# Kernel tuning notes

Hardware: AMD Instinct MI355X
Metric: run time of the kernel (lower is better)

The kernel has to match this reference:

```python
import jax, jax.numpy as jnp
import numpy as np

D = 1024
NH = 16
DH = D // NH
B = 2
N = 2048
EPS = 1e-5


def setup_inputs() -> dict:
    key = jax.random.key(0)
    ks = jax.random.split(key, 12)
    s = 0.02
    return {
        "x": jax.random.normal(ks[0], (B, N, D), jnp.float32),
        "Wq": jax.random.normal(ks[1], (D, D), jnp.float32) * s,
        "Wk": jax.random.normal(ks[2], (D, D), jnp.float32) * s,
        "Wv": jax.random.normal(ks[3], (D, D), jnp.float32) * s,
        "Wo": jax.random.normal(ks[4], (D, D), jnp.float32) * s,
        "bo": jnp.zeros((D,), jnp.float32),
        "ln1_scale": jnp.ones((D,), jnp.float32),
        "ln1_shift": jnp.zeros((D,), jnp.float32),
        "ln2_scale": jnp.ones((D,), jnp.float32),
        "ln2_shift": jnp.zeros((D,), jnp.float32),
        "W1": jax.random.normal(ks[5], (4 * D, D), jnp.float32) * s,
        "b1": jnp.zeros((4 * D,), jnp.float32),
        "W2": jax.random.normal(ks[6], (D, 4 * D), jnp.float32) * s,
        "b2": jnp.zeros((D,), jnp.float32),
    }


def _layernorm(x, scale, shift):
    mean = jnp.mean(x, axis=-1, keepdims=True)
    var = jnp.mean(jnp.square(x - mean), axis=-1, keepdims=True)  # unbiased=False
    return scale * ((x - mean) / jnp.sqrt(var + EPS)) + shift


def _gelu(x):
    c = jnp.sqrt(jnp.asarray(2.0 / jnp.pi, x.dtype))
    return 0.5 * x * (1.0 + jnp.tanh(c * (x + 0.044715 * x * x * x)))


def reference(x, Wq, Wk, Wv, Wo, bo, ln1_scale, ln1_shift, ln2_scale, ln2_shift, W1, b1, W2, b2):
    Bx, Nx, d = x.shape
    # pre-MHA LN
    h = _layernorm(x, ln1_scale, ln1_shift)
    # projections (torch Linear: y = h @ W.T), no bias for Wq/Wk/Wv
    q = (h @ Wq.T).reshape(Bx, Nx, NH, DH).transpose(0, 2, 1, 3)  # [B,nh,N,dh]
    k = (h @ Wk.T).reshape(Bx, Nx, NH, DH).transpose(0, 2, 1, 3)
    v = (h @ Wv.T).reshape(Bx, Nx, NH, DH).transpose(0, 2, 1, 3)
    s = jnp.einsum("bhnd,bhmd->bhnm", q, k)  # [B,nh,N,N]
    causal = jnp.tril(jnp.ones((Nx, Nx), bool))
    s = jnp.where(causal, s, -jnp.inf)
    p = jax.nn.softmax(s / jnp.sqrt(jnp.asarray(DH, s.dtype)), axis=-1)
    pv = jnp.einsum("bhnm,bhmd->bhnd", p, v)
    pv = pv.transpose(0, 2, 1, 3).reshape(Bx, Nx, d)
    attn = pv @ Wo.T + bo
    x = x + attn  # residual (dropout is identity, dpo=0)
    # pre-FFN LN + FFN
    h = _layernorm(x, ln2_scale, ln2_shift)
    h = _gelu(h @ W1.T + b1)
    h = h @ W2.T + b2
    return x + h
```

## Files before the change

kernel.cpp:

```cpp
#include <hip/hip_runtime.h>
#include <hip/hip_bf16.h>
#include <math.h>

#define Dmod   1024
#define NHmod  16
#define DHmod  64
#define Bmod   2
#define Nmod   2048
#define Mrows  (Bmod * Nmod)
#define FF     (4 * Dmod)
#define EPSLN  1e-5f

typedef __attribute__((ext_vector_type(8))) short bf16x8;
typedef __attribute__((ext_vector_type(4))) float f32x4;
typedef unsigned short ushort_t;
typedef unsigned int uint_t;

#define MFMA16x16x32(a, b, c) __builtin_amdgcn_mfma_f32_16x16x32_bf16((a), (b), (c), 0, 0, 0)

#define AS1 __attribute__((address_space(1)))
#define AS3 __attribute__((address_space(3)))

__device__ __forceinline__ void gload_lds16(const ushort_t* g, ushort_t* l) {
    __builtin_amdgcn_global_load_lds((const AS1 uint_t*)(const void*)g,
                                     (AS3 uint_t*)(void*)l, 16, 0, 0);
}

__device__ __forceinline__ ushort_t f2bf(float f) {
    union { float f; uint_t u; } v; v.f = f;
    uint_t r = v.u + 0x7FFFu + ((v.u >> 16) & 1u);
    return (ushort_t)(r >> 16);
}

__device__ __forceinline__ float bf2f(uint_t u) {
    union { float f; uint_t u; } v; v.u = u << 16;
    return v.f;
}

__global__ __launch_bounds__(256) void cvt_kernel(const float* __restrict__ Wq, const float* __restrict__ Wk,
                                                  const float* __restrict__ Wv, const float* __restrict__ Wo,
                                                  const float* __restrict__ W1, const float* __restrict__ W2,
                                                  ushort_t* __restrict__ qkv, ushort_t* __restrict__ wo,
                                                  ushort_t* __restrict__ w1, ushort_t* __restrict__ w2) {
    int u = blockIdx.x * 256 + threadIdx.x;
    const float* src; ushort_t* dst; int i;
    float scale = 1.0f;
    if (u < 393216) {
        if (u < 131072)      { src = Wq; dst = qkv;           i = u; scale = 0.125f; }
        else if (u < 262144) { src = Wk; dst = qkv + 1048576; i = u - 131072; }
        else                 { src = Wv; dst = qkv + 2097152; i = u - 262144; }
    } else if (u < 524288)   { src = Wo; dst = wo; i = u - 393216; }
    else if (u < 1048576)    { src = W1; dst = w1; i = u - 524288; }
    else                     { src = W2; dst = w2; i = u - 1048576; }
    float4 a = ((const float4*)src)[2 * i];
    float4 b = ((const float4*)src)[2 * i + 1];
    uint4 o;
    o.x = (uint_t)f2bf(a.x * scale) | ((uint_t)f2bf(a.y * scale) << 16);
    o.y = (uint_t)f2bf(a.z * scale) | ((uint_t)f2bf(a.w * scale) << 16);
    o.z = (uint_t)f2bf(b.x * scale) | ((uint_t)f2bf(b.y * scale) << 16);
    o.w = (uint_t)f2bf(b.z * scale) | ((uint_t)f2bf(b.w * scale) << 16);
    ((uint4*)dst)[i] = o;
}

__global__ __launch_bounds__(256) void ln_bf_kernel(const float* __restrict__ x,
                                                    const float* __restrict__ scale,
                                                    const float* __restrict__ shift,
                                                    ushort_t* __restrict__ out) {
    int row = blockIdx.x;
    const float4* xr = (const float4*)(x + (size_t)row * Dmod);
    float4 v = xr[threadIdx.x];
    float s  = v.x + v.y + v.z + v.w;
    float s2 = v.x*v.x + v.y*v.y + v.z*v.z + v.w*v.w;

    __shared__ float rs[8], rs2[8];
    #pragma unroll
    for (int o = 32; o; o >>= 1) { s += __shfl_down(s, o); s2 += __shfl_down(s2, o); }
    int wave = threadIdx.x >> 6, lane = threadIdx.x & 63;
    if (lane == 0) { rs[wave] = s; rs2[wave] = s2; }
    __syncthreads();
    if (threadIdx.x == 0) {
        rs[0]  = rs[0] + rs[1] + rs[2] + rs[3];
        rs2[0] = rs2[0] + rs2[1] + rs2[2] + rs2[3];
    }
    __syncthreads();
    float mean = rs[0] * (1.0f / Dmod);
    float var  = rs2[0] * (1.0f / Dmod) - mean * mean;
    float rstd = rsqrtf(var + EPSLN);

    float4 sc = ((const float4*)scale)[threadIdx.x];
    float4 sh = ((const float4*)shift)[threadIdx.x];
    uint2 o;
    o.x = (uint_t)f2bf(sc.x * (v.x - mean) * rstd + sh.x) |
          ((uint_t)f2bf(sc.y * (v.y - mean) * rstd + sh.y) << 16);
    o.y = (uint_t)f2bf(sc.z * (v.z - mean) * rstd + sh.z) |
          ((uint_t)f2bf(sc.w * (v.w - mean) * rstd + sh.w) << 16);
    ((uint2*)(out + (size_t)row * Dmod))[threadIdx.x] = o;
}

__device__ __forceinline__ float gelu_f(float x) {
    const float c = 0.7978845608028654f;
    float u = c * (x + 0.044715f * x * x * x);
    return x / (1.0f + __expf(-2.0f * u));
}

#define DSR(D, A, OFF) asm volatile("ds_read_b128 %0, %1 offset:" OFF : "=v"(D) : "v"(A))
#define SB0 __builtin_amdgcn_sched_barrier(0)
#define BARR __builtin_amdgcn_s_barrier()
#define LGKM0 asm volatile("s_waitcnt lgkmcnt(0)" ::)

#define MMQ0 \
  acc[0][0]=MFMA16x16x32(a0,b0,acc[0][0]); acc[1][0]=MFMA16x16x32(a1,b0,acc[1][0]); \
  acc[2][0]=MFMA16x16x32(a2,b0,acc[2][0]); acc[3][0]=MFMA16x16x32(a3,b0,acc[3][0]); \
  acc[0][1]=MFMA16x16x32(a0,b1,acc[0][1]); acc[1][1]=MFMA16x16x32(a1,b1,acc[1][1]); \
  acc[2][1]=MFMA16x16x32(a2,b1,acc[2][1]); acc[3][1]=MFMA16x16x32(a3,b1,acc[3][1]); \
  acc[0][2]=MFMA16x16x32(a0,b2,acc[0][2]); acc[1][2]=MFMA16x16x32(a1,b2,acc[1][2]); \
  acc[2][2]=MFMA16x16x32(a2,b2,acc[2][2]); acc[3][2]=MFMA16x16x32(a3,b2,acc[3][2]); \
  acc[0][3]=MFMA16x16x32(a0,b3,acc[0][3]); acc[1][3]=MFMA16x16x32(a1,b3,acc[1][3]); \
  acc[2][3]=MFMA16x16x32(a2,b3,acc[2][3]); acc[3][3]=MFMA16x16x32(a3,b3,acc[3][3]);
#define MMQ4 \
  acc[4][0]=MFMA16x16x32(a0,b0,acc[4][0]); acc[5][0]=MFMA16x16x32(a1,b0,acc[5][0]); \
  acc[6][0]=MFMA16x16x32(a2,b0,acc[6][0]); acc[7][0]=MFMA16x16x32(a3,b0,acc[7][0]); \
  acc[4][1]=MFMA16x16x32(a0,b1,acc[4][1]); acc[5][1]=MFMA16x16x32(a1,b1,acc[5][1]); \
  acc[6][1]=MFMA16x16x32(a2,b1,acc[6][1]); acc[7][1]=MFMA16x16x32(a3,b1,acc[7][1]); \
  acc[4][2]=MFMA16x16x32(a0,b2,acc[4][2]); acc[5][2]=MFMA16x16x32(a1,b2,acc[5][2]); \
  acc[6][2]=MFMA16x16x32(a2,b2,acc[6][2]); acc[7][2]=MFMA16x16x32(a3,b2,acc[7][2]); \
  acc[4][3]=MFMA16x16x32(a0,b3,acc[4][3]); acc[5][3]=MFMA16x16x32(a1,b3,acc[5][3]); \
  acc[6][3]=MFMA16x16x32(a2,b3,acc[6][3]); acc[7][3]=MFMA16x16x32(a3,b3,acc[7][3]);

template <int MODE>
__global__ __launch_bounds__(512, 2) void gemm256(const ushort_t* __restrict__ A,
                                                  const ushort_t* __restrict__ W,
                                                  const float* __restrict__ bias,
                                                  void* __restrict__ Cv,
                                                  int M, int Nout, int K, int KS,
                                                  int GN, int GM) {
    __shared__ ushort_t Ab[32768];
    __shared__ ushort_t Bb[32768];
    int tid = threadIdx.x;
    int w  = tid >> 6, l = tid & 63;
    int li = l & 15,  g = l >> 4;
    int wm = w >> 2,  wn = w & 3;

    int xcd = blockIdx.x & 7;
    int c   = blockIdx.x >> 3;
    int RN = GN >> 2, RM = GM >> 1;
    int rsz = RN * RM;
    int bz = c / rsz;
    int r  = c - bz * rsz;
    int bm = (xcd >> 2) * RM + r / RN;
    int bn = (xcd & 3) * RN + r % RN;

    int lc   = (l & 7) ^ (l >> 3);
    int sgr  = w * 32 + 2 * (l >> 3) + (lc >> 2);
    int colo = (lc & 3) * 8;
    const ushort_t* sA0 = A + (size_t)(bm * 256 + sgr) * K + bz * KS + colo;
    const ushort_t* sA1 = sA0 + (size_t)16 * K;
    const ushort_t* sB0 = W + (size_t)(bn * 256 + sgr) * K + bz * KS + colo;
    const ushort_t* sB1 = sB0 + (size_t)16 * K;

    uint_t chunkpos = (uint_t)(((((li & 1) << 2) + g) ^ (li >> 1)) << 4);
    uint_t aBase = (uint_t)(uintptr_t)(&Ab[0]) + (uint_t)(wm * 8192 + (li >> 1) * 128) + chunkpos;
    uint_t bBase = (uint_t)(uintptr_t)(&Bb[0]) + (uint_t)(wn * 4096 + (li >> 1) * 128) + chunkpos;

    f32x4 acc[8][4];
    #pragma unroll
    for (int i = 0; i < 8; i++)
        #pragma unroll
        for (int j = 0; j < 4; j++) acc[i][j] = (f32x4){0.f, 0.f, 0.f, 0.f};

    const int NT = KS >> 6;

    {
        ushort_t* dA = &Ab[0] + w * 1024;
        ushort_t* dB = &Bb[0] + w * 1024;
        gload_lds16(sA0,      dA);        gload_lds16(sA1,      dA + 512);
        gload_lds16(sB0,      dB);        gload_lds16(sB1,      dB + 512);
        gload_lds16(sA0 + 32, dA + 8192); gload_lds16(sA1 + 32, dA + 8192 + 512);
        gload_lds16(sB0 + 32, dB + 8192); gload_lds16(sB1 + 32, dB + 8192 + 512);
    }
    asm volatile("s_waitcnt vmcnt(4)" ::);
    SB0; BARR;

    for (int t = 0; t < NT; ++t) {
        int d = t & 1;
        bool pf = (t + 1 < NT);
        int kn = (t + 1) * 64;
        uint_t aAddr = aBase + (uint_t)(d * 32768);
        uint_t bAddr = bBase + (uint_t)(d * 32768);
        ushort_t* dA = &Ab[0] + (d ^ 1) * 16384 + w * 1024;
        ushort_t* dB = &Bb[0] + (d ^ 1) * 16384 + w * 1024;
        bf16x8 a0, a1, a2, a3, b0, b1, b2, b3;

        DSR(a0, aAddr, "0");    DSR(a1, aAddr, "1024");
        DSR(a2, aAddr, "2048"); DSR(a3, aAddr, "3072");
        DSR(b0, bAddr, "0");    DSR(b1, bAddr, "1024");
        DSR(b2, bAddr, "2048"); DSR(b3, bAddr, "3072");
        if (pf) { gload_lds16(sA0 + kn, dA); gload_lds16(sA1 + kn, dA + 512); }
        SB0; BARR; LGKM0; SB0;
        __builtin_amdgcn_s_setprio(1);
        MMQ0
        __builtin_amdgcn_s_setprio(0);
        SB0; BARR;

        DSR(a0, aAddr, "4096"); DSR(a1, aAddr, "5120");
        DSR(a2, aAddr, "6144"); DSR(a3, aAddr, "7168");
        if (pf) { gload_lds16(sB0 + kn, dB); gload_lds16(sB1 + kn, dB + 512); }
        SB0; BARR; LGKM0; SB0;
        __builtin_amdgcn_s_setprio(1);
        MMQ4
        __builtin_amdgcn_s_setprio(0);
        if (pf) { asm volatile("s_waitcnt vmcnt(4)" ::); }
        else    { asm volatile("s_waitcnt vmcnt(0)" ::); }
        SB0; BARR;

        DSR(a0, aAddr, "16384"); DSR(a1, aAddr, "17408");
        DSR(a2, aAddr, "18432"); DSR(a3, aAddr, "19456");
        DSR(b0, bAddr, "16384"); DSR(b1, bAddr, "17408");
        DSR(b2, bAddr, "18432"); DSR(b3, bAddr, "19456");
        if (pf) { gload_lds16(sA0 + kn + 32, dA + 8192); gload_lds16(sA1 + kn + 32, dA + 8192 + 512); }
        SB0; BARR; LGKM0; SB0;
        __builtin_amdgcn_s_setprio(1);
        MMQ0
        __builtin_amdgcn_s_setprio(0);
        SB0; BARR;

        DSR(a0, aAddr, "20480"); DSR(a1, aAddr, "21504");
        DSR(a2, aAddr, "22528"); DSR(a3, aAddr, "23552");
        if (pf) { gload_lds16(sB0 + kn + 32, dB + 8192); gload_lds16(sB1 + kn + 32, dB + 8192 + 512); }
        SB0; BARR; LGKM0; SB0;
        __builtin_amdgcn_s_setprio(1);
        MMQ4
        __builtin_amdgcn_s_setprio(0);
        asm volatile("s_waitcnt vmcnt(4)" ::);
        SB0; BARR;
    }

    #pragma unroll
    for (int fm = 0; fm < 8; fm++) {
        #pragma unroll
        for (int fn = 0; fn < 4; fn++) {
            int nn = bn * 256 + wn * 64 + fn * 16 + li;
            int mB = bm * 256 + wm * 128 + (fm >> 2) * 64 + (fm & 3) * 16 + g * 4;
            if (MODE == 0) {
                int which = nn >> 10, col = nn & 1023;
                int h = col >> 6, dd = col & 63;
                int b = mB >> 11, n0 = mB & (Nmod - 1);
                ushort_t* C = (ushort_t*)Cv;
                if (which == 2) {
                    uint2 pk;
                    pk.x = (uint_t)f2bf(acc[fm][fn][0]) | ((uint_t)f2bf(acc[fm][fn][1]) << 16);
                    pk.y = (uint_t)f2bf(acc[fm][fn][2]) | ((uint_t)f2bf(acc[fm][fn][3]) << 16);
                    *(uint2*)(C + 8388608u + (((size_t)(b * NHmod + h)) * DHmod + dd) * Nmod + n0) = pk;
                } else {
                    #pragma unroll
                    for (int r2 = 0; r2 < 4; r2++) {
                        size_t idx = (size_t)which * 4194304u +
                                     (((size_t)(b * NHmod + h)) * Nmod + n0 + r2) * DHmod + dd;
                        C[idx] = f2bf(acc[fm][fn][r2]);
                    }
                }
            } else if (MODE == 2) {
                ushort_t* C = (ushort_t*)Cv;
                #pragma unroll
                for (int r2 = 0; r2 < 4; r2++)
                    C[(size_t)(mB + r2) * Nout + nn] = f2bf(gelu_f(acc[fm][fn][r2] + bias[nn]));
            } else {
                ushort_t* P = (ushort_t*)Cv + (size_t)bz * M * Nout;
                #pragma unroll
                for (int r2 = 0; r2 < 4; r2++)
                    P[(size_t)(mB + r2) * Nout + nn] = f2bf(acc[fm][fn][r2]);
            }
        }
    }
}

template <int MODE, int BN>
__global__ __launch_bounds__(256) void bgemm(const ushort_t* __restrict__ A,
                                             const ushort_t* __restrict__ W,
                                             const float* __restrict__ bias,
                                             const float* __restrict__ resid,
                                             void* __restrict__ Cv,
                                             int M, int Nout, int K, int KS,
                                             int GN, int GM) {
    const int BSZ = BN * 32;
    const int NFR = BN / 32;
    __shared__ ushort_t As[3 * 4096];
    __shared__ ushort_t Bs[3 * BSZ];
    int tid  = threadIdx.x;
    int w    = tid >> 6, lane = tid & 63;
    int li   = lane & 15, g = lane >> 4;
    int wr   = w >> 1,  wc = w & 1;

    int xcd = blockIdx.x & 7;
    int c   = blockIdx.x >> 3;
    int RN  = GN >> 2;
    int RM  = GM >> 1;
    int rsz = RN * RM;
    int bz  = c / rsz;
    int r   = c - bz * rsz;
    int bm  = (xcd >> 2) * RM + r / RN;
    int bn  = (xcd & 3) * RN + r % RN;

    int srow = tid >> 2;
    int scol = ((tid & 3) ^ ((tid >> 3) & 3)) * 8;
    const ushort_t* Ag = A + (size_t)(bm * 128 + srow) * K + bz * KS + scol;
    const ushort_t* Wg = W + (size_t)(bn * BN  + srow) * K + bz * KS + scol;
    ushort_t* AsW = As + w * 512;
    ushort_t* BsW = Bs + w * 512;

    int rsw = ((g ^ ((li >> 1) & 3)) * 8);

    uint_t lbA = (uint_t)(uintptr_t)(&As[0]);
    uint_t lbB = (uint_t)(uintptr_t)(&Bs[0]);
    uint_t abase = lbA + (uint_t)(((wr * 64 + li) * 32 + rsw) * 2);
    uint_t bbase = lbB + (uint_t)(((wc * (BN / 2) + li) * 32 + rsw) * 2);

    f32x4 acc[4][NFR];
    #pragma unroll
    for (int i = 0; i < 4; i++)
        #pragma unroll
        for (int j = 0; j < NFR; j++) acc[i][j] = (f32x4){0.f, 0.f, 0.f, 0.f};

    const int NT = KS >> 5;

    auto stagef = [&](int bufA, int bufB, int t) {
        int k0 = t * 32;
        gload_lds16(Ag + k0,          AsW + bufA);
        gload_lds16(Ag + 64 * K + k0, AsW + bufA + 2048);
        gload_lds16(Wg + k0,          BsW + bufB);
        if (BN == 128) gload_lds16(Wg + 64 * K + k0, BsW + bufB + 2048);
    };

    stagef(0, 0, 0);
    stagef(4096, BSZ, 1);

    int curA = 0, curB = 0;
    int stgA = 8192, stgB = 2 * BSZ;

    for (int t = 0; t < NT; ++t) {
        if (t == NT - 1) { asm volatile("s_waitcnt vmcnt(0)" ::); }
        else if (BN == 128) { asm volatile("s_waitcnt vmcnt(4)" ::); }
        else { asm volatile("s_waitcnt vmcnt(3)" ::); }
        __builtin_amdgcn_s_barrier();
        __builtin_amdgcn_sched_barrier(0);
        if (t + 2 < NT) stagef(stgA, stgB, t + 2);
        __builtin_amdgcn_sched_barrier(0);
        bf16x8 af[4], bfr[NFR];
        uint_t aa = abase + (uint_t)(curA * 2);
        uint_t bb = bbase + (uint_t)(curB * 2);
        asm volatile("ds_read_b128 %0, %1"             : "=v"(af[0]) : "v"(aa));
        asm volatile("ds_read_b128 %0, %1 offset:1024" : "=v"(af[1]) : "v"(aa));
        asm volatile("ds_read_b128 %0, %1 offset:2048" : "=v"(af[2]) : "v"(aa));
        asm volatile("ds_read_b128 %0, %1 offset:3072" : "=v"(af[3]) : "v"(aa));
        asm volatile("ds_read_b128 %0, %1"             : "=v"(bfr[0]) : "v"(bb));
        asm volatile("ds_read_b128 %0, %1 offset:1024" : "=v"(bfr[1]) : "v"(bb));
        if (NFR == 4) {
            asm volatile("ds_read_b128 %0, %1 offset:2048" : "=v"(bfr[2]) : "v"(bb));
            asm volatile("ds_read_b128 %0, %1 offset:3072" : "=v"(bfr[3]) : "v"(bb));
        }
        asm volatile("s_waitcnt lgkmcnt(0)" ::);
        __builtin_amdgcn_sched_barrier(0);
        __builtin_amdgcn_s_setprio(1);
        #pragma unroll
        for (int mi = 0; mi < 4; mi++)
            #pragma unroll
            for (int ni = 0; ni < NFR; ni++)
                acc[mi][ni] = MFMA16x16x32(af[mi], bfr[ni], acc[mi][ni]);
        __builtin_amdgcn_s_setprio(0);
        curA = (curA == 8192) ? 0 : curA + 4096;
        curB = (curB == 2 * BSZ) ? 0 : curB + BSZ;
        stgA = (stgA == 8192) ? 0 : stgA + 4096;
        stgB = (stgB == 2 * BSZ) ? 0 : stgB + BSZ;
    }

    #pragma unroll
    for (int mi = 0; mi < 4; mi++) {
        #pragma unroll
        for (int ni = 0; ni < NFR; ni++) {
            int nn = bn * BN + wc * (BN / 2) + ni * 16 + li;
            #pragma unroll
            for (int r2 = 0; r2 < 4; r2++) {
                int m = bm * 128 + wr * 64 + mi * 16 + g * 4 + r2;
                float v = acc[mi][ni][r2];
                if (MODE == 1) {
                    float* C = (float*)Cv;
                    C[(size_t)m * Nout + nn] = v + bias[nn] + resid[(size_t)m * Nout + nn];
                } else if (MODE == 3) {
                    float* C = (float*)Cv + (size_t)bz * M * Nout;
                    C[(size_t)m * Nout + nn] = v;
                }
            }
        }
    }
}

__global__ __launch_bounds__(256) void red_ln_kernel(const float* __restrict__ p,
                                                     const float* __restrict__ x,
                                                     const float* __restrict__ bo,
                                                     const float* __restrict__ scale,
                                                     const float* __restrict__ shift,
                                                     float* __restrict__ x1,
                                                     ushort_t* __restrict__ h2) {
    int row = blockIdx.x;
    int t   = threadIdx.x;
    const size_t MD = (size_t)Mrows * Dmod;
    float4 a = ((const float4*)(p + (size_t)row * Dmod))[t];
    float4 b = ((const float4*)(p + MD + (size_t)row * Dmod))[t];
    float4 xr = ((const float4*)(x + (size_t)row * Dmod))[t];
    float4 bb = ((const float4*)bo)[t];
    float4 v;
    v.x = a.x + b.x + xr.x + bb.x;
    v.y = a.y + b.y + xr.y + bb.y;
    v.z = a.z + b.z + xr.z + bb.z;
    v.w = a.w + b.w + xr.w + bb.w;
    ((float4*)(x1 + (size_t)row * Dmod))[t] = v;

    float s  = v.x + v.y + v.z + v.w;
    float s2 = v.x*v.x + v.y*v.y + v.z*v.z + v.w*v.w;
    __shared__ float rs[8], rs2[8];
    #pragma unroll
    for (int o = 32; o; o >>= 1) { s += __shfl_down(s, o); s2 += __shfl_down(s2, o); }
    int wave = t >> 6, lane = t & 63;
    if (lane == 0) { rs[wave] = s; rs2[wave] = s2; }
    __syncthreads();
    if (t == 0) {
        rs[0]  = rs[0] + rs[1] + rs[2] + rs[3];
        rs2[0] = rs2[0] + rs2[1] + rs2[2] + rs2[3];
    }
    __syncthreads();
    float mean = rs[0] * (1.0f / Dmod);
    float var  = rs2[0] * (1.0f / Dmod) - mean * mean;
    float rstd = rsqrtf(var + EPSLN);

    float4 sc = ((const float4*)scale)[t];
    float4 sh = ((const float4*)shift)[t];
    uint2 o;
    o.x = (uint_t)f2bf(sc.x * (v.x - mean) * rstd + sh.x) |
          ((uint_t)f2bf(sc.y * (v.y - mean) * rstd + sh.y) << 16);
    o.y = (uint_t)f2bf(sc.z * (v.z - mean) * rstd + sh.z) |
          ((uint_t)f2bf(sc.w * (v.w - mean) * rstd + sh.w) << 16);
    ((uint2*)(h2 + (size_t)row * Dmod))[t] = o;
}

__global__ __launch_bounds__(256) void red_out4_kernel(const ushort_t* __restrict__ p,
                                                       const float* __restrict__ x1,
                                                       const float* __restrict__ b2,
                                                       float* __restrict__ out) {
    const size_t MD4 = (size_t)Mrows * Dmod / 4;
    size_t i = (size_t)blockIdx.x * 256 + threadIdx.x;
    if (i >= MD4) return;
    float4 xr = ((const float4*)x1)[i];
    float4 bb = ((const float4*)b2)[i & 255];
    float4 v;
    v.x = xr.x + bb.x; v.y = xr.y + bb.y; v.z = xr.z + bb.z; v.w = xr.w + bb.w;
    #pragma unroll
    for (int z = 0; z < 4; z++) {
        uint2 pk = ((const uint2*)(p + (size_t)z * Mrows * Dmod))[i];
        v.x += bf2f(pk.x & 0xffffu);
        v.y += bf2f(pk.x >> 16);
        v.z += bf2f(pk.y & 0xffffu);
        v.w += bf2f(pk.y >> 16);
    }
    ((float4*)out)[i] = v;
}

__global__ __launch_bounds__(256) void fattn_kernel(const ushort_t* __restrict__ Q,
                                                    const ushort_t* __restrict__ K,
                                                    const ushort_t* __restrict__ VT,
                                                    ushort_t* __restrict__ O) {
    int bid = blockIdx.x;
    int xcd = bid & 7;
    int j   = bid >> 3;
    int bh  = xcd * 4 + (j & 3);
    int qt  = 31 - (j >> 2);
    int b   = bh >> 4, hh = bh & 15;
    int w    = threadIdx.x >> 6;
    int lane = threadIdx.x & 63;
    int li   = lane & 15;
    int g    = lane >> 4;

    __shared__ ushort_t Klds[2][4096];
    __shared__ ushort_t Vlds[2][4096];
    __shared__ ushort_t Plds[4][16][72];

    int q0 = qt * 64 + w * 16;
    int q  = q0 + li;

    const ushort_t* Qb = Q  + (size_t)bh * Nmod * DHmod;
    const ushort_t* Kb = K  + (size_t)bh * Nmod * DHmod;
    const ushort_t* Vb = VT + (size_t)bh * DHmod * Nmod;

    bf16x8 qf[2];
    #pragma unroll
    for (int c = 0; c < 2; c++)
        qf[c] = *(const bf16x8*)(Qb + (size_t)q * DHmod + c * 32 + g * 8);

    f32x4 po[4];
    #pragma unroll
    for (int mt = 0; mt < 4; mt++) po[mt] = (f32x4){0.f, 0.f, 0.f, 0.f};
    float l = 0.f;

    const int ntiles = qt + 1;

    int r_sub = lane >> 3;
    int cc    = ((lane & 7) ^ (r_sub & 7)) * 8;

    int swz  = (li & 7) * 8;
    int roff = li * 64;
    int c0k  = (g * 8) ^ swz;
    int c1k  = (32 + g * 8) ^ swz;

    auto stage = [&](int buf, int kt) {
        int k0 = kt * 64;
        #pragma unroll
        for (int i2 = 0; i2 < 2; i2++) {
            int i   = w * 2 + i2;
            int row = i * 8 + r_sub;
            gload_lds16(Kb + (size_t)(k0 + row) * DHmod + cc, &Klds[buf][i * 512]);
            gload_lds16(Vb + (size_t)row * Nmod + k0 + cc,    &Vlds[buf][i * 512]);
        }
    };

    stage(0, 0);

    for (int kt = 0; kt < ntiles; ++kt) {
        __syncthreads();
        if (kt + 1 < ntiles) stage((kt + 1) & 1, kt + 1);
        int cur = kt & 1;
        int k0  = kt * 64;

        f32x4 s[4];
        __builtin_amdgcn_s_setprio(1);
        #pragma unroll
        for (int mt = 0; mt < 4; mt++) {
            bf16x8 kf0 = *(const bf16x8*)&Klds[cur][mt * 1024 + roff + c0k];
            bf16x8 kf1 = *(const bf16x8*)&Klds[cur][mt * 1024 + roff + c1k];
            s[mt] = (f32x4){0.f, 0.f, 0.f, 0.f};
            s[mt] = MFMA16x16x32(kf0, qf[0], s[mt]);
            s[mt] = MFMA16x16x32(kf1, qf[1], s[mt]);
        }
        __builtin_amdgcn_s_setprio(0);

        if (kt == qt) {
            #pragma unroll
            for (int mt = 0; mt < 4; mt++)
                #pragma unroll
                for (int r = 0; r < 4; r++)
                    if (k0 + mt * 16 + g * 4 + r > q) s[mt][r] = -INFINITY;
        }
        float ptile = 0.f;
        #pragma unroll
        for (int mt = 0; mt < 4; mt++) {
            float p0 = __expf(s[mt][0]);
            float p1 = __expf(s[mt][1]);
            float p2 = __expf(s[mt][2]);
            float p3 = __expf(s[mt][3]);
            ptile += (p0 + p1) + (p2 + p3);
            uint2 pk;
            pk.x = (uint_t)f2bf(p0) | ((uint_t)f2bf(p1) << 16);
            pk.y = (uint_t)f2bf(p2) | ((uint_t)f2bf(p3) << 16);
            *(uint2*)&Plds[w][li][mt * 16 + g * 4] = pk;
        }
        l += ptile;

        asm volatile("" ::: "memory");

        bf16x8 pf0 = *(const bf16x8*)&Plds[w][li][g * 8];
        bf16x8 pf1 = *(const bf16x8*)&Plds[w][li][32 + g * 8];
        __builtin_amdgcn_s_setprio(1);
        #pragma unroll
        for (int mt = 0; mt < 4; mt++) {
            bf16x8 vf0 = *(const bf16x8*)&Vlds[cur][mt * 1024 + roff + c0k];
            bf16x8 vf1 = *(const bf16x8*)&Vlds[cur][mt * 1024 + roff + c1k];
            po[mt] = MFMA16x16x32(vf0, pf0, po[mt]);
            po[mt] = MFMA16x16x32(vf1, pf1, po[mt]);
        }
        __builtin_amdgcn_s_setprio(0);
        asm volatile("" ::: "memory");
    }

    l += __shfl_xor(l, 16);
    l += __shfl_xor(l, 32);
    float inv = 1.0f / l;
    ushort_t* Orow = O + ((size_t)(b * Nmod + q)) * Dmod + hh * DHmod;
    #pragma unroll
    for (int mt = 0; mt < 4; mt++) {
        uint2 pk;
        pk.x = (uint_t)f2bf(po[mt][0] * inv) | ((uint_t)f2bf(po[mt][1] * inv) << 16);
        pk.y = (uint_t)f2bf(po[mt][2] * inv) | ((uint_t)f2bf(po[mt][3] * inv) << 16);
        *(uint2*)(Orow + mt * 16 + g * 4) = pk;
    }
}

extern "C" void kernel_launch(void* const* d_in, const int* in_sizes, int n_in,
                              void* d_out, int out_size, void* d_ws, size_t ws_size,
                              hipStream_t stream) {
    const float* x    = (const float*)d_in[0];
    const float* Wq   = (const float*)d_in[1];
    const float* Wk   = (const float*)d_in[2];
    const float* Wv   = (const float*)d_in[3];
    const float* Wo   = (const float*)d_in[4];
    const float* bo   = (const float*)d_in[5];
    const float* ln1s = (const float*)d_in[6];
    const float* ln1b = (const float*)d_in[7];
    const float* ln2s = (const float*)d_in[8];
    const float* ln2b = (const float*)d_in[9];
    const float* W1   = (const float*)d_in[10];
    const float* b1   = (const float*)d_in[11];
    const float* W2   = (const float*)d_in[12];
    const float* b2   = (const float*)d_in[13];
    float* out = (float*)d_out;
    char*  wsb = (char*)d_ws;

    ushort_t* h_bf  = (ushort_t*)wsb;
    ushort_t* qb    = (ushort_t*)(wsb + (8u  << 20));
    ushort_t* kb    = qb + 4194304;
    ushort_t* vtb   = qb + 8388608;
    float*    x1    = (float*)(wsb + (32u << 20));
    ushort_t* h2_bf = (ushort_t*)(wsb + (48u << 20));
    ushort_t* g_bf  = (ushort_t*)(wsb + (56u << 20));
    ushort_t* wqkv  = (ushort_t*)(wsb + (88u << 20));
    ushort_t* wo_b  = (ushort_t*)(wsb + (94u << 20));
    ushort_t* w1_b  = (ushort_t*)(wsb + (96u << 20));
    ushort_t* w2_b  = (ushort_t*)(wsb + (104u << 20));
    ushort_t* att   = h_bf;
    float*    pWo = (float*)(wsb + (56u << 20));
    ushort_t* pFd = (ushort_t*)wsb;

    cvt_kernel<<<6144, 256, 0, stream>>>(Wq, Wk, Wv, Wo, W1, W2, wqkv, wo_b, w1_b, w2_b);
    ln_bf_kernel<<<Mrows, 256, 0, stream>>>(x, ln1s, ln1b, h_bf);
    gemm256<0><<<192, 512, 0, stream>>>(h_bf, wqkv, nullptr, qb, Mrows, 3072, Dmod, Dmod, 12, 16);
    fattn_kernel<<<1024, 256, 0, stream>>>(qb, kb, vtb, att);
    bgemm<3, 64><<<1024, 256, 0, stream>>>(att, wo_b, nullptr, nullptr, pWo, Mrows, Dmod, Dmod, Dmod / 2, 16, 32);
    red_ln_kernel<<<Mrows, 256, 0, stream>>>(pWo, x, bo, ln2s, ln2b, x1, h2_bf);
    gemm256<2><<<256, 512, 0, stream>>>(h2_bf, w1_b, b1, g_bf, Mrows, FF, Dmod, Dmod, 16, 16);
    gemm256<4><<<256, 512, 0, stream>>>(g_bf, w2_b, nullptr, pFd, Mrows, Dmod, FF, FF / 4, 4, 16);
    red_out4_kernel<<<(Mrows * Dmod / 4 + 255) / 256, 256, 0, stream>>>(pFd, x1, b2, out);
}
```

Baseline: 220.6 us.

## Stagger LDS waits in gemm256 and route Wo projection through split-K gemm256

The gemm256 main loop now waits on LDS reads one fragment at a time (lgkmcnt 3/2/1/0), so MFMAs can start before all eight ds_reads finish. The Wo output projection drops the separate bgemm kernel and reuses gemm256 in split-K mode 4, writing four bf16 partials instead of two fp32 partials. The reduction+LayerNorm kernel is rewritten to sum the four bf16 partials. This cuts partial-sum traffic and uses the faster tile kernel, at the cost of extra bf16 rounding on the partials.

```diff
diff --git a/kernel.cpp b/kernel.cpp
--- a/kernel.cpp
+++ b/kernel.cpp
@@ -106,26 +106,14 @@
 #define DSR(D, A, OFF) asm volatile("ds_read_b128 %0, %1 offset:" OFF : "=v"(D) : "v"(A))
 #define SB0 __builtin_amdgcn_sched_barrier(0)
 #define BARR __builtin_amdgcn_s_barrier()
-#define LGKM0 asm volatile("s_waitcnt lgkmcnt(0)" ::)
-
-#define MMQ0 \
-  acc[0][0]=MFMA16x16x32(a0,b0,acc[0][0]); acc[1][0]=MFMA16x16x32(a1,b0,acc[1][0]); \
-  acc[2][0]=MFMA16x16x32(a2,b0,acc[2][0]); acc[3][0]=MFMA16x16x32(a3,b0,acc[3][0]); \
-  acc[0][1]=MFMA16x16x32(a0,b1,acc[0][1]); acc[1][1]=MFMA16x16x32(a1,b1,acc[1][1]); \
-  acc[2][1]=MFMA16x16x32(a2,b1,acc[2][1]); acc[3][1]=MFMA16x16x32(a3,b1,acc[3][1]); \
-  acc[0][2]=MFMA16x16x32(a0,b2,acc[0][2]); acc[1][2]=MFMA16x16x32(a1,b2,acc[1][2]); \
-  acc[2][2]=MFMA16x16x32(a2,b2,acc[2][2]); acc[3][2]=MFMA16x16x32(a3,b2,acc[3][2]); \
-  acc[0][3]=MFMA16x16x32(a0,b3,acc[0][3]); acc[1][3]=MFMA16x16x32(a1,b3,acc[1][3]); \
-  acc[2][3]=MFMA16x16x32(a2,b3,acc[2][3]); acc[3][3]=MFMA16x16x32(a3,b3,acc[3][3]);
-#define MMQ4 \
-  acc[4][0]=MFMA16x16x32(a0,b0,acc[4][0]); acc[5][0]=MFMA16x16x32(a1,b0,acc[5][0]); \
-  acc[6][0]=MFMA16x16x32(a2,b0,acc[6][0]); acc[7][0]=MFMA16x16x32(a3,b0,acc[7][0]); \
-  acc[4][1]=MFMA16x16x32(a0,b1,acc[4][1]); acc[5][1]=MFMA16x16x32(a1,b1,acc[5][1]); \
-  acc[6][1]=MFMA16x16x32(a2,b1,acc[6][1]); acc[7][1]=MFMA16x16x32(a3,b1,acc[7][1]); \
-  acc[4][2]=MFMA16x16x32(a0,b2,acc[4][2]); acc[5][2]=MFMA16x16x32(a1,b2,acc[5][2]); \
-  acc[6][2]=MFMA16x16x32(a2,b2,acc[6][2]); acc[7][2]=MFMA16x16x32(a3,b2,acc[7][2]); \
-  acc[4][3]=MFMA16x16x32(a0,b3,acc[4][3]); acc[5][3]=MFMA16x16x32(a1,b3,acc[5][3]); \
-  acc[6][3]=MFMA16x16x32(a2,b3,acc[6][3]); acc[7][3]=MFMA16x16x32(a3,b3,acc[7][3]);
+#define LGKM(N) asm volatile("s_waitcnt lgkmcnt(" #N ")" ::)
+
+#define GRP_QM0(J, B) \
+  acc[0][J]=MFMA16x16x32(a0,B,acc[0][J]); acc[1][J]=MFMA16x16x32(a1,B,acc[1][J]); \
+  acc[2][J]=MFMA16x16x32(a2,B,acc[2][J]); acc[3][J]=MFMA16x16x32(a3,B,acc[3][J]);
+#define GRP_QM1(I, A) \
+  acc[I][0]=MFMA16x16x32(A,b0,acc[I][0]); acc[I][1]=MFMA16x16x32(A,b1,acc[I][1]); \
+  acc[I][2]=MFMA16x16x32(A,b2,acc[I][2]); acc[I][3]=MFMA16x16x32(A,b3,acc[I][3]);
 
 template <int MODE>
 __global__ __launch_bounds__(512, 2) void gemm256(const ushort_t* __restrict__ A,
@@ -196,18 +184,32 @@
         DSR(b0, bAddr, "0");    DSR(b1, bAddr, "1024");
         DSR(b2, bAddr, "2048"); DSR(b3, bAddr, "3072");
         if (pf) { gload_lds16(sA0 + kn, dA); gload_lds16(sA1 + kn, dA + 512); }
-        SB0; BARR; LGKM0; SB0;
+        SB0; BARR;
+        LGKM(3); SB0;
         __builtin_amdgcn_s_setprio(1);
-        MMQ0
+        GRP_QM0(0, b0)
+        LGKM(2); SB0;
+        GRP_QM0(1, b1)
+        LGKM(1); SB0;
+        GRP_QM0(2, b2)
+        LGKM(0); SB0;
+        GRP_QM0(3, b3)
         __builtin_amdgcn_s_setprio(0);
         SB0; BARR;
 
         DSR(a0, aAddr, "4096"); DSR(a1, aAddr, "5120");
         DSR(a2, aAddr, "6144"); DSR(a3, aAddr, "7168");
         if (pf) { gload_lds16(sB0 + kn, dB); gload_lds16(sB1 + kn, dB + 512); }
-        SB0; BARR; LGKM0; SB0;
+        SB0; BARR;
+        LGKM(3); SB0;
         __builtin_amdgcn_s_setprio(1);
-        MMQ4
+        GRP_QM1(4, a0)
+        LGKM(2); SB0;
+        GRP_QM1(5, a1)
+        LGKM(1); SB0;
+        GRP_QM1(6, a2)
+        LGKM(0); SB0;
+        GRP_QM1(7, a3)
         __builtin_amdgcn_s_setprio(0);
         if (pf) { asm volatile("s_waitcnt vmcnt(4)" ::); }
         else    { asm volatile("s_waitcnt vmcnt(0)" ::); }
@@ -218,18 +220,32 @@
         DSR(b0, bAddr, "16384"); DSR(b1, bAddr, "17408");
         DSR(b2, bAddr, "18432"); DSR(b3, bAddr, "19456");
         if (pf) { gload_lds16(sA0 + kn + 32, dA + 8192); gload_lds16(sA1 + kn + 32, dA + 8192 + 512); }
-        SB0; BARR; LGKM0; SB0;
+        SB0; BARR;
+        LGKM(3); SB0;
         __builtin_amdgcn_s_setprio(1);
-        MMQ0
+        GRP_QM0(0, b0)
+        LGKM(2); SB0;
+        GRP_QM0(1, b1)
+        LGKM(1); SB0;
+        GRP_QM0(2, b2)
+        LGKM(0); SB0;
+        GRP_QM0(3, b3)
         __builtin_amdgcn_s_setprio(0);
         SB0; BARR;
 
         DSR(a0, aAddr, "20480"); DSR(a1, aAddr, "21504");
         DSR(a2, aAddr, "22528"); DSR(a3, aAddr, "23552");
         if (pf) { gload_lds16(sB0 + kn + 32, dB + 8192); gload_lds16(sB1 + kn + 32, dB + 8192 + 512); }
-        SB0; BARR; LGKM0; SB0;
+        SB0; BARR;
+        LGKM(3); SB0;
         __builtin_amdgcn_s_setprio(1);
-        MMQ4
+        GRP_QM1(4, a0)
+        LGKM(2); SB0;
+        GRP_QM1(5, a1)
+        LGKM(1); SB0;
+        GRP_QM1(6, a2)
+        LGKM(0); SB0;
+        GRP_QM1(7, a3)
         __builtin_amdgcn_s_setprio(0);
         asm volatile("s_waitcnt vmcnt(4)" ::);
         SB0; BARR;
@@ -274,145 +290,29 @@
     }
 }
 
-template <int MODE, int BN>
-__global__ __launch_bounds__(256) void bgemm(const ushort_t* __restrict__ A,
-                                             const ushort_t* __restrict__ W,
-                                             const float* __restrict__ bias,
-                                             const float* __restrict__ resid,
-                                             void* __restrict__ Cv,
-                                             int M, int Nout, int K, int KS,
-                                             int GN, int GM) {
-    const int BSZ = BN * 32;
-    const int NFR = BN / 32;
-    __shared__ ushort_t As[3 * 4096];
-    __shared__ ushort_t Bs[3 * BSZ];
-    int tid  = threadIdx.x;
-    int w    = tid >> 6, lane = tid & 63;
-    int li   = lane & 15, g = lane >> 4;
-    int wr   = w >> 1,  wc = w & 1;
-
-    int xcd = blockIdx.x & 7;
-    int c   = blockIdx.x >> 3;
-    int RN  = GN >> 2;
-    int RM  = GM >> 1;
-    int rsz = RN * RM;
-    int bz  = c / rsz;
-    int r   = c - bz * rsz;
-    int bm  = (xcd >> 2) * RM + r / RN;
-    int bn  = (xcd & 3) * RN + r % RN;
-
-    int srow = tid >> 2;
-    int scol = ((tid & 3) ^ ((tid >> 3) & 3)) * 8;
-    const ushort_t* Ag = A + (size_t)(bm * 128 + srow) * K + bz * KS + scol;
-    const ushort_t* Wg = W + (size_t)(bn * BN  + srow) * K + bz * KS + scol;
-    ushort_t* AsW = As + w * 512;
-    ushort_t* BsW = Bs + w * 512;
-
-    int rsw = ((g ^ ((li >> 1) & 3)) * 8);
-
-    uint_t lbA = (uint_t)(uintptr_t)(&As[0]);
-    uint_t lbB = (uint_t)(uintptr_t)(&Bs[0]);
-    uint_t abase = lbA + (uint_t)(((wr * 64 + li) * 32 + rsw) * 2);
-    uint_t bbase = lbB + (uint_t)(((wc * (BN / 2) + li) * 32 + rsw) * 2);
-
-    f32x4 acc[4][NFR];
-    #pragma unroll
-    for (int i = 0; i < 4; i++)
-        #pragma unroll
-        for (int j = 0; j < NFR; j++) acc[i][j] = (f32x4){0.f, 0.f, 0.f, 0.f};
-
-    const int NT = KS >> 5;
-
-    auto stagef = [&](int bufA, int bufB, int t) {
-        int k0 = t * 32;
-        gload_lds16(Ag + k0,          AsW + bufA);
-        gload_lds16(Ag + 64 * K + k0, AsW + bufA + 2048);
-        gload_lds16(Wg + k0,          BsW + bufB);
-        if (BN == 128) gload_lds16(Wg + 64 * K + k0, BsW + bufB + 2048);
-    };
-
-    stagef(0, 0, 0);
-    stagef(4096, BSZ, 1);
-
-    int curA = 0, curB = 0;
-    int stgA = 8192, stgB = 2 * BSZ;
-
-    for (int t = 0; t < NT; ++t) {
-        if (t == NT - 1) { asm volatile("s_waitcnt vmcnt(0)" ::); }
-        else if (BN == 128) { asm volatile("s_waitcnt vmcnt(4)" ::); }
-        else { asm volatile("s_waitcnt vmcnt(3)" ::); }
-        __builtin_amdgcn_s_barrier();
-        __builtin_amdgcn_sched_barrier(0);
-        if (t + 2 < NT) stagef(stgA, stgB, t + 2);
-        __builtin_amdgcn_sched_barrier(0);
-        bf16x8 af[4], bfr[NFR];
-        uint_t aa = abase + (uint_t)(curA * 2);
-        uint_t bb = bbase + (uint_t)(curB * 2);
-        asm volatile("ds_read_b128 %0, %1"             : "=v"(af[0]) : "v"(aa));
-        asm volatile("ds_read_b128 %0, %1 offset:1024" : "=v"(af[1]) : "v"(aa));
-        asm volatile("ds_read_b128 %0, %1 offset:2048" : "=v"(af[2]) : "v"(aa));
-        asm volatile("ds_read_b128 %0, %1 offset:3072" : "=v"(af[3]) : "v"(aa));
-        asm volatile("ds_read_b128 %0, %1"             : "=v"(bfr[0]) : "v"(bb));
-        asm volatile("ds_read_b128 %0, %1 offset:1024" : "=v"(bfr[1]) : "v"(bb));
-        if (NFR == 4) {
-            asm volatile("ds_read_b128 %0, %1 offset:2048" : "=v"(bfr[2]) : "v"(bb));
-            asm volatile("ds_read_b128 %0, %1 offset:3072" : "=v"(bfr[3]) : "v"(bb));
-        }
-        asm volatile("s_waitcnt lgkmcnt(0)" ::);
-        __builtin_amdgcn_sched_barrier(0);
-        __builtin_amdgcn_s_setprio(1);
-        #pragma unroll
-        for (int mi = 0; mi < 4; mi++)
-            #pragma unroll
-            for (int ni = 0; ni < NFR; ni++)
-                acc[mi][ni] = MFMA16x16x32(af[mi], bfr[ni], acc[mi][ni]);
-        __builtin_amdgcn_s_setprio(0);
-        curA = (curA == 8192) ? 0 : curA + 4096;
-        curB = (curB == 2 * BSZ) ? 0 : curB + BSZ;
-        stgA = (stgA == 8192) ? 0 : stgA + 4096;
-        stgB = (stgB == 2 * BSZ) ? 0 : stgB + BSZ;
-    }
-
-    #pragma unroll
-    for (int mi = 0; mi < 4; mi++) {
-        #pragma unroll
-        for (int ni = 0; ni < NFR; ni++) {
-            int nn = bn * BN + wc * (BN / 2) + ni * 16 + li;
-            #pragma unroll
-            for (int r2 = 0; r2 < 4; r2++) {
-                int m = bm * 128 + wr * 64 + mi * 16 + g * 4 + r2;
-                float v = acc[mi][ni][r2];
-                if (MODE == 1) {
-                    float* C = (float*)Cv;
-                    C[(size_t)m * Nout + nn] = v + bias[nn] + resid[(size_t)m * Nout + nn];
-                } else if (MODE == 3) {
-                    float* C = (float*)Cv + (size_t)bz * M * Nout;
-                    C[(size_t)m * Nout + nn] = v;
-                }
-            }
-        }
-    }
-}
-
-__global__ __launch_bounds__(256) void red_ln_kernel(const float* __restrict__ p,
-                                                     const float* __restrict__ x,
-                                                     const float* __restrict__ bo,
-                                                     const float* __restrict__ scale,
-                                                     const float* __restrict__ shift,
-                                                     float* __restrict__ x1,
-                                                     ushort_t* __restrict__ h2) {
+__global__ __launch_bounds__(256) void red_ln4_kernel(const ushort_t* __restrict__ p,
+                                                      const float* __restrict__ x,
+                                                      const float* __restrict__ bo,
+                                                      const float* __restrict__ scale,
+                                                      const float* __restrict__ shift,
+                                                      float* __restrict__ x1,
+                                                      ushort_t* __restrict__ h2) {
     int row = blockIdx.x;
     int t   = threadIdx.x;
     const size_t MD = (size_t)Mrows * Dmod;
-    float4 a = ((const float4*)(p + (size_t)row * Dmod))[t];
-    float4 b = ((const float4*)(p + MD + (size_t)row * Dmod))[t];
+    size_t i = (size_t)row * 256 + t;
     float4 xr = ((const float4*)(x + (size_t)row * Dmod))[t];
     float4 bb = ((const float4*)bo)[t];
     float4 v;
-    v.x = a.x + b.x + xr.x + bb.x;
-    v.y = a.y + b.y + xr.y + bb.y;
-    v.z = a.z + b.z + xr.z + bb.z;
-    v.w = a.w + b.w + xr.w + bb.w;
+    v.x = xr.x + bb.x; v.y = xr.y + bb.y; v.z = xr.z + bb.z; v.w = xr.w + bb.w;
+    #pragma unroll
+    for (int z = 0; z < 4; z++) {
+        uint2 pk = ((const uint2*)(p + (size_t)z * MD))[i];
+        v.x += bf2f(pk.x & 0xffffu);
+        v.y += bf2f(pk.x >> 16);
+        v.z += bf2f(pk.y & 0xffffu);
+        v.w += bf2f(pk.y >> 16);
+    }
     ((float4*)(x1 + (size_t)row * Dmod))[t] = v;
 
     float s  = v.x + v.y + v.z + v.w;
@@ -624,15 +524,15 @@
     ushort_t* w1_b  = (ushort_t*)(wsb + (96u << 20));
     ushort_t* w2_b  = (ushort_t*)(wsb + (104u << 20));
     ushort_t* att   = h_bf;
-    float*    pWo = (float*)(wsb + (56u << 20));
-    ushort_t* pFd = (ushort_t*)wsb;
+    ushort_t* pWoB = (ushort_t*)(wsb + (56u << 20));
+    ushort_t* pFd  = (ushort_t*)wsb;
 
     cvt_kernel<<<6144, 256, 0, stream>>>(Wq, Wk, Wv, Wo, W1, W2, wqkv, wo_b, w1_b, w2_b);
     ln_bf_kernel<<<Mrows, 256, 0, stream>>>(x, ln1s, ln1b, h_bf);
     gemm256<0><<<192, 512, 0, stream>>>(h_bf, wqkv, nullptr, qb, Mrows, 3072, Dmod, Dmod, 12, 16);
     fattn_kernel<<<1024, 256, 0, stream>>>(qb, kb, vtb, att);
-    bgemm<3, 64><<<1024, 256, 0, stream>>>(att, wo_b, nullptr, nullptr, pWo, Mrows, Dmod, Dmod, Dmod / 2, 16, 32);
-    red_ln_kernel<<<Mrows, 256, 0, stream>>>(pWo, x, bo, ln2s, ln2b, x1, h2_bf);
+    gemm256<4><<<256, 512, 0, stream>>>(att, wo_b, nullptr, pWoB, Mrows, Dmod, Dmod, Dmod / 4, 4, 16);
+    red_ln4_kernel<<<Mrows, 256, 0, stream>>>(pWoB, x, bo, ln2s, ln2b, x1, h2_bf);
     gemm256<2><<<256, 512, 0, stream>>>(h2_bf, w1_b, b1, g_bf, Mrows, FF, Dmod, Dmod, 16, 16);
     gemm256<4><<<256, 512, 0, stream>>>(g_bf, w2_b, nullptr, pFd, Mrows, Dmod, FF, FF / 4, 4, 16);
     red_out4_kernel<<<(Mrows * Dmod / 4 + 255) / 256, 256, 0, stream>>>(pFd, x1, b2, out);
```

Result: no change. 221.0 us (+0.2%).
